# Kernel optimization log

Hardware: AMD Instinct MI355X
Metric: run time of the kernel (lower is better)

The kernel has to match this reference:

```python
import jax, jax.numpy as jnp
import numpy as np

N, M, F = 16384, 16384, 512
NUM_BATCHES = 16


def setup_inputs() -> dict:
    key = jax.random.key(0)
    k1, k2, k3, k4 = jax.random.split(key, 4)
    H_q = jax.random.normal(k1, (N, F), dtype=jnp.float32)
    H_c = jax.random.normal(k2, (M, F), dtype=jnp.float32)
    batch_q = jnp.sort(jax.random.randint(k3, (N,), 0, NUM_BATCHES, dtype=jnp.int64))
    batch_c = jnp.sort(jax.random.randint(k4, (M,), 0, NUM_BATCHES, dtype=jnp.int64))
    return {"H_q": H_q, "H_c": H_c, "batch_q": batch_q, "batch_c": batch_c}


def reference(H_q, H_c, batch_q, batch_c):
    # scores: [n, m] dense dot-product similarity
    scores = jnp.matmul(H_q, H_c.T)
    # mask[i, j] = True iff query i and candidate j belong to the same batch element
    mask = batch_q[:, None] == batch_c[None, :]
    out = jnp.where(mask, scores, -jnp.inf)
    return out, mask
```

## Files before the change

### kernel.cpp

```cpp
#include <hip/hip_runtime.h>
#include <hip/hip_bf16.h>
#include <math.h>


#define BM 128
#define BN 128
#define NEG_BIG (-3.3895313892515355e+38f)

typedef float    f32x4  __attribute__((ext_vector_type(4)));
typedef unsigned u32x4  __attribute__((ext_vector_type(4)));
typedef short    short8 __attribute__((ext_vector_type(8)));

__device__ __forceinline__ unsigned pk2(float a, float b) {
    unsigned ua = __builtin_bit_cast(unsigned, a);
    unsigned ub = __builtin_bit_cast(unsigned, b);
    return (ub & 0xFFFF0000u) | (ua >> 16);
}

__global__ __launch_bounds__(256) void dot_tile_kernel(
    const float* __restrict__ Hq, const float* __restrict__ Hc,
    const int* __restrict__ bq, const int* __restrict__ bc,
    float* __restrict__ out, float* __restrict__ mask_out,
    int M, int F, int ntx, int write_mask)
{
    const int t   = threadIdx.x;
    const int bid = blockIdx.x;
    const int i0  = (bid / ntx) * BM;
    const int j0  = (bid % ntx) * BN;

    if (!(bq[i0] <= bc[j0 + BN - 1] && bc[j0] <= bq[i0 + BM - 1])) {
        const f32x4 m4 = (f32x4){NEG_BIG, NEG_BIG, NEG_BIG, NEG_BIG};
        const f32x4 z4 = (f32x4){0.f, 0.f, 0.f, 0.f};
        #pragma unroll
        for (int v = 0; v < 16; ++v) {
            const int idx = t + v * 256;
            const int r   = idx >> 5;
            const int c4  = idx & 31;
            const size_t off = (size_t)(i0 + r) * M + j0 + c4 * 4;
            *(f32x4*)(out + off) = m4;
            if (write_mask) *(f32x4*)(mask_out + off) = z4;
        }
        return;
    }

    __shared__ char SM[4 * 1088 * 4];
    __shared__ int bql[BM];
    __shared__ int bcl[BN];

    char*  Ab = SM;
    char*  Bb = SM + 8192;
    float* tb = (float*)SM;

    if (t < BM) bql[t] = bq[i0 + t];
    else        bcl[t - BM] = bc[j0 + (t - BM)];

    f32x4 acc[4][4];
    #pragma unroll
    for (int a = 0; a < 4; ++a)
        #pragma unroll
        for (int b = 0; b < 4; ++b) acc[a][b] = (f32x4){0.f, 0.f, 0.f, 0.f};

    const int l   = t & 63;
    const int wid = t >> 6;
    const int wr  = wid >> 1;
    const int wc  = wid & 1;
    const int lg  = l >> 4;
    const int lm  = l & 15;

    const int sr  = t >> 1;
    const int scf = (t & 1) * 16;
    const int swW = ((sr >> 1) & 3) << 4;
    const int wb0 = sr * 64 + (t & 1) * 32;
    const int swR = ((lm >> 1) & 3) << 4;

    const float* aptr = Hq + (size_t)(i0 + sr) * F + scf;
    const float* bptr = Hc + (size_t)(j0 + sr) * F + scf;

    const int nks = F >> 5;

    f32x4 cA[4], cB[4];
    #pragma unroll
    for (int u = 0; u < 4; ++u) {
        cA[u] = *(const f32x4*)(aptr + u * 4);
        cB[u] = *(const f32x4*)(bptr + u * 4);
    }

    #pragma unroll 2
    for (int ks = 0; ks < nks; ++ks) {
        f32x4 nA[4], nB[4];
        const bool last = (ks == nks - 1);
        if (!last) {
            const int k1 = (ks + 1) * 32;
            #pragma unroll
            for (int u = 0; u < 4; ++u) {
                nA[u] = *(const f32x4*)(aptr + k1 + u * 4);
                nB[u] = *(const f32x4*)(bptr + k1 + u * 4);
            }
        }
        __syncthreads();
        u32x4 pa0 = (u32x4){pk2(cA[0][0],cA[0][1]), pk2(cA[0][2],cA[0][3]),
                            pk2(cA[1][0],cA[1][1]), pk2(cA[1][2],cA[1][3])};
        u32x4 pa1 = (u32x4){pk2(cA[2][0],cA[2][1]), pk2(cA[2][2],cA[2][3]),
                            pk2(cA[3][0],cA[3][1]), pk2(cA[3][2],cA[3][3])};
        u32x4 pb0 = (u32x4){pk2(cB[0][0],cB[0][1]), pk2(cB[0][2],cB[0][3]),
                            pk2(cB[1][0],cB[1][1]), pk2(cB[1][2],cB[1][3])};
        u32x4 pb1 = (u32x4){pk2(cB[2][0],cB[2][1]), pk2(cB[2][2],cB[2][3]),
                            pk2(cB[3][0],cB[3][1]), pk2(cB[3][2],cB[3][3])};
        *(u32x4*)(Ab + ((wb0     ) ^ swW)) = pa0;
        *(u32x4*)(Ab + ((wb0 + 16) ^ swW)) = pa1;
        *(u32x4*)(Bb + ((wb0     ) ^ swW)) = pb0;
        *(u32x4*)(Bb + ((wb0 + 16) ^ swW)) = pb1;
        __syncthreads();
        short8 af[4], bf[4];
        #pragma unroll
        for (int m = 0; m < 4; ++m) {
            const int arow = wr * 64 + m * 16 + lm;
            af[m] = *(const short8*)(Ab + arow * 64 + ((lg * 16) ^ swR));
            const int brow = wc * 64 + m * 16 + lm;
            bf[m] = *(const short8*)(Bb + brow * 64 + ((lg * 16) ^ swR));
        }
        #pragma unroll
        for (int m = 0; m < 4; ++m)
            #pragma unroll
            for (int n = 0; n < 4; ++n)
                acc[m][n] = __builtin_amdgcn_mfma_f32_16x16x32_bf16(
                    af[m], bf[n], acc[m][n], 0, 0, 0);
        if (!last) {
            #pragma unroll
            for (int u = 0; u < 4; ++u) { cA[u] = nA[u]; cB[u] = nB[u]; }
        }
    }

    __syncthreads();
    const int r_loc = l >> 2;
    const int sl    = l & 3;
    #pragma unroll
    for (int m = 0; m < 4; ++m) {
        #pragma unroll
        for (int n = 0; n < 4; ++n)
            #pragma unroll
            for (int v = 0; v < 4; ++v)
                tb[wid * 1088 + (lg * 4 + v) * 68 + n * 16 + lm] = acc[m][n][v];
        __syncthreads();
        const int row = wr * 64 + m * 16 + r_loc;
        const int bqv = bql[row];
        const size_t rowoff = (size_t)(i0 + row) * M + j0;
        #pragma unroll
        for (int q = 0; q < 4; ++q) {
            const int slot = sl + q * 4;
            const int c    = wc * 64 + slot * 4;
            f32x4 vv = *(f32x4*)&tb[wid * 1088 + r_loc * 68 + slot * 4];
            f32x4 vo, vm;
            #pragma unroll
            for (int j = 0; j < 4; ++j) {
                const bool eq = (bqv == bcl[c + j]);
                vo[j] = eq ? vv[j] : NEG_BIG;
                vm[j] = eq ? 1.0f : 0.0f;
            }
            *(f32x4*)(out + rowoff + c) = vo;
            if (write_mask) *(f32x4*)(mask_out + rowoff + c) = vm;
        }
        __syncthreads();
    }
}

extern "C" void kernel_launch(void* const* d_in, const int* in_sizes, int n_in,
                              void* d_out, int out_size, void* d_ws, size_t ws_size,
                              hipStream_t stream) {
    const float* Hq = (const float*)d_in[0];
    const float* Hc = (const float*)d_in[1];
    const int*   bq = (const int*)d_in[2];
    const int*   bc = (const int*)d_in[3];

    const int N = in_sizes[2];
    const int M = in_sizes[3];
    const int F = in_sizes[0] / N;

    float* out = (float*)d_out;
    const long long NM = (long long)N * M;
    const int write_mask = ((long long)out_size >= 2 * NM) ? 1 : 0;
    float* mask_out = out + NM;

    const int nty = N / BM;
    const int ntx = M / BN;

    dot_tile_kernel<<<nty * ntx, 256, 0, stream>>>(
        Hq, Hc, bq, bc, out, mask_out, M, F, ntx, write_mask);
}
```

Measured before the change: 481.1 us.

## Split masked fill into separate row kernel using binary-searched batch ranges

The tile kernel now returns early for tiles with no overlapping batches and, in overlapping tiles, writes only the in-batch columns. Per-row column ranges come from binary searches over the sorted batch_c. A second kernel fills everything outside each row's [lo,hi) range with the masked value and zero mask, writing each output element exactly once. The aim is to avoid redundant per-element compares and shorten the tile kernel. It relies on sorted batch arrays, adds a second launch, and uses scalar stores at range edges.

```diff
diff --git a/kernel.cpp b/kernel.cpp
--- a/kernel.cpp
+++ b/kernel.cpp
@@ -11,10 +11,59 @@
 typedef unsigned u32x4  __attribute__((ext_vector_type(4)));
 typedef short    short8 __attribute__((ext_vector_type(8)));
 
+__device__ __forceinline__ int lbound(const int* __restrict__ a, int n, int v) {
+    int lo = 0, hi = n;
+    while (lo < hi) { int mid = (lo + hi) >> 1; if (a[mid] < v) lo = mid + 1; else hi = mid; }
+    return lo;
+}
+__device__ __forceinline__ int ubound(const int* __restrict__ a, int n, int v) {
+    int lo = 0, hi = n;
+    while (lo < hi) { int mid = (lo + hi) >> 1; if (a[mid] <= v) lo = mid + 1; else hi = mid; }
+    return lo;
+}
 __device__ __forceinline__ unsigned pk2(float a, float b) {
     unsigned ua = __builtin_bit_cast(unsigned, a);
     unsigned ub = __builtin_bit_cast(unsigned, b);
     return (ub & 0xFFFF0000u) | (ua >> 16);
+}
+
+__global__ __launch_bounds__(256) void fill_rows_kernel(
+    const int* __restrict__ bq, const int* __restrict__ bc,
+    float* __restrict__ out, float* __restrict__ mask_out,
+    int M, int write_mask)
+{
+    const int i = blockIdx.x;
+    const int t = threadIdx.x;
+    const int b  = bq[i];
+    const int lo = lbound(bc, M, b);
+    const int hi = ubound(bc, M, b);
+
+    const f32x4 m4 = (f32x4){NEG_BIG, NEG_BIG, NEG_BIG, NEG_BIG};
+    const f32x4 z4 = (f32x4){0.f, 0.f, 0.f, 0.f};
+    float* po = out + (size_t)i * M;
+    float* pm = mask_out + (size_t)i * M;
+
+    const int lo4 = lo >> 2;
+    for (int x = t; x < lo4; x += 256) {
+        *(f32x4*)(po + x * 4) = m4;
+        if (write_mask) *(f32x4*)(pm + x * 4) = z4;
+    }
+    if (t < (lo & 3)) {
+        po[lo4 * 4 + t] = NEG_BIG;
+        if (write_mask) pm[lo4 * 4 + t] = 0.f;
+    }
+    int nhead = (4 - (hi & 3)) & 3;
+    if (nhead > M - hi) nhead = M - hi;
+    if (t < nhead) {
+        po[hi + t] = NEG_BIG;
+        if (write_mask) pm[hi + t] = 0.f;
+    }
+    const int h4 = (hi + 3) >> 2;
+    const int m4cnt = M >> 2;
+    for (int x = h4 + t; x < m4cnt; x += 256) {
+        *(f32x4*)(po + x * 4) = m4;
+        if (write_mask) *(f32x4*)(pm + x * 4) = z4;
+    }
 }
 
 __global__ __launch_bounds__(256) void dot_tile_kernel(
@@ -28,31 +77,20 @@
     const int i0  = (bid / ntx) * BM;
     const int j0  = (bid % ntx) * BN;
 
-    if (!(bq[i0] <= bc[j0 + BN - 1] && bc[j0] <= bq[i0 + BM - 1])) {
-        const f32x4 m4 = (f32x4){NEG_BIG, NEG_BIG, NEG_BIG, NEG_BIG};
-        const f32x4 z4 = (f32x4){0.f, 0.f, 0.f, 0.f};
-        #pragma unroll
-        for (int v = 0; v < 16; ++v) {
-            const int idx = t + v * 256;
-            const int r   = idx >> 5;
-            const int c4  = idx & 31;
-            const size_t off = (size_t)(i0 + r) * M + j0 + c4 * 4;
-            *(f32x4*)(out + off) = m4;
-            if (write_mask) *(f32x4*)(mask_out + off) = z4;
-        }
-        return;
-    }
+    if (!(bq[i0] <= bc[j0 + BN - 1] && bc[j0] <= bq[i0 + BM - 1])) return;
 
     __shared__ char SM[4 * 1088 * 4];
-    __shared__ int bql[BM];
-    __shared__ int bcl[BN];
+    __shared__ int slo[BM], shi[BM];
 
     char*  Ab = SM;
     char*  Bb = SM + 8192;
     float* tb = (float*)SM;
 
-    if (t < BM) bql[t] = bq[i0 + t];
-    else        bcl[t - BM] = bc[j0 + (t - BM)];
+    if (t < BM) {
+        const int b = bq[i0 + t];
+        slo[t] = lbound(bc, M, b);
+        shi[t] = ubound(bc, M, b);
+    }
 
     f32x4 acc[4][4];
     #pragma unroll
@@ -134,6 +172,7 @@
     __syncthreads();
     const int r_loc = l >> 2;
     const int sl    = l & 3;
+    const f32x4 one4 = (f32x4){1.f, 1.f, 1.f, 1.f};
     #pragma unroll
     for (int m = 0; m < 4; ++m) {
         #pragma unroll
@@ -143,22 +182,27 @@
                 tb[wid * 1088 + (lg * 4 + v) * 68 + n * 16 + lm] = acc[m][n][v];
         __syncthreads();
         const int row = wr * 64 + m * 16 + r_loc;
-        const int bqv = bql[row];
+        const int cl  = max(slo[row] - j0, 0);
+        const int ch  = min(shi[row] - j0, BN);
         const size_t rowoff = (size_t)(i0 + row) * M + j0;
         #pragma unroll
         for (int q = 0; q < 4; ++q) {
             const int slot = sl + q * 4;
             const int c    = wc * 64 + slot * 4;
             f32x4 vv = *(f32x4*)&tb[wid * 1088 + r_loc * 68 + slot * 4];
-            f32x4 vo, vm;
-            #pragma unroll
-            for (int j = 0; j < 4; ++j) {
-                const bool eq = (bqv == bcl[c + j]);
-                vo[j] = eq ? vv[j] : NEG_BIG;
-                vm[j] = eq ? 1.0f : 0.0f;
+            if (c >= cl && c + 4 <= ch) {
+                *(f32x4*)(out + rowoff + c) = vv;
+                if (write_mask) *(f32x4*)(mask_out + rowoff + c) = one4;
+            } else if (c + 4 > cl && c < ch) {
+                #pragma unroll
+                for (int j = 0; j < 4; ++j) {
+                    const int cc = c + j;
+                    if (cc >= cl && cc < ch) {
+                        out[rowoff + cc] = vv[j];
+                        if (write_mask) mask_out[rowoff + cc] = 1.0f;
+                    }
+                }
             }
-            *(f32x4*)(out + rowoff + c) = vo;
-            if (write_mask) *(f32x4*)(mask_out + rowoff + c) = vm;
         }
         __syncthreads();
     }
@@ -186,4 +230,6 @@
 
     dot_tile_kernel<<<nty * ntx, 256, 0, stream>>>(
         Hq, Hc, bq, bc, out, mask_out, M, F, ntx, write_mask);
-}
+    fill_rows_kernel<<<N, 256, 0, stream>>>(
+        bq, bc, out, mask_out, M, write_mask);
+}
```

Result: slower. 547.9 us (+13.9%).
